# Performance work log

Hardware: AMD Instinct MI355X
Metric: run time of the kernel (lower is better)

Reference implementation:

```python
import jax, jax.numpy as jnp
import numpy as np

EPS = 1e-5


def setup_inputs() -> dict:
    key = jax.random.key(0)
    k1, k2, k3, k4 = jax.random.split(key, 4)
    B, C, H, W = 32, 256, 64, 64
    x_real = jax.random.normal(k1, (B, C, H, W), dtype=jnp.float32)
    x_imag = jax.random.normal(k2, (B, C, H, W), dtype=jnp.float32)
    # per-channel 2x2 affine weight and 2-vector bias (module init is
    # 0.7071*I and zeros; we perturb so gradients are non-trivial)
    weight = (0.70710678 * jnp.eye(2, dtype=jnp.float32)[:, :, None]
              + 0.05 * jax.random.normal(k3, (2, 2, C), dtype=jnp.float32))
    bias = 0.05 * jax.random.normal(k4, (2, C), dtype=jnp.float32)
    return {"x_real": x_real, "x_imag": x_imag, "weight": weight, "bias": bias}


def reference(x_real, x_imag, weight, bias):
    # Complex BatchNorm (training-mode batch statistics).
    # x_*: [B, C, H, W]; stats reduced over (B, H, W) per channel C.
    axes = (0, 2, 3)
    mu_r = jnp.mean(x_real, axes)  # [C]
    mu_i = jnp.mean(x_imag, axes)  # [C]
    xr = x_real - mu_r[None, :, None, None]
    xi = x_imag - mu_i[None, :, None, None]

    # 2x2 covariance per channel, eps on the diagonal
    Vrr = jnp.mean(xr * xr, axes) + EPS  # [C]
    Vii = jnp.mean(xi * xi, axes) + EPS  # [C]
    Vri = jnp.mean(xr * xi, axes)        # [C]

    # Analytic inverse square root of the 2x2 SPD matrix [[Vrr,Vri],[Vri,Vii]]
    s = jnp.sqrt(Vrr * Vii - Vri * Vri)       # sqrt(det)
    t = jnp.sqrt(Vrr + Vii + 2.0 * s)         # sqrt(trace + 2 sqrt(det))
    inv_st = 1.0 / (s * t)
    Rrr = (Vii + s) * inv_st
    Rii = (Vrr + s) * inv_st
    Rri = -Vri * inv_st

    # Whitening (per-channel 2x2 matmul on (real, imag))
    cb = lambda v: v[None, :, None, None]
    xhat_r = cb(Rrr) * xr + cb(Rri) * xi
    xhat_i = cb(Rri) * xr + cb(Rii) * xi

    # Affine: out = W @ xhat + b, W: [2,2,C], b: [2,C]
    out_r = cb(weight[0, 0]) * xhat_r + cb(weight[0, 1]) * xhat_i + cb(bias[0])
    out_i = cb(weight[1, 0]) * xhat_r + cb(weight[1, 1]) * xhat_i + cb(bias[1])
    return jnp.stack([out_r, out_i], axis=0)  # [2, B, C, H, W]
```

## Files before the change

### kernel.cpp

```cpp
#include <hip/hip_runtime.h>
#include <math.h>

#define C_CH   256
#define HW     4096
#define B_N    32
#define N_PER_CH (B_N * HW)
#define N_TOT  ((size_t)B_N * C_CH * HW)
#define EPS_BN 1e-5f

#define NT 512
#define RS 22
#define LS 9

typedef float f32x4 __attribute__((ext_vector_type(4)));

__device__ __forceinline__ unsigned pk(float a, float b) {
    unsigned ua = __float_as_uint(a);
    unsigned ub = __float_as_uint(b);
    ua += 0x7fffu + ((ua >> 16) & 1u);
    ub += 0x7fffu + ((ub >> 16) & 1u);
    return (ua >> 16) | (ub & 0xffff0000u);
}
__device__ __forceinline__ float blo(unsigned p) { return __uint_as_float(p << 16); }
__device__ __forceinline__ float bhi(unsigned p) { return __uint_as_float(p & 0xffff0000u); }

__global__ __launch_bounds__(NT, 2) void cbn_bf16ret3(
    const float* __restrict__ xr, const float* __restrict__ xi,
    const float* __restrict__ weight,
    const float* __restrict__ bias,
    float* __restrict__ out)
{
    const int c = blockIdx.x;
    const int t = threadIdx.x;

    const f32x4* r4 = reinterpret_cast<const f32x4*>(xr);
    const f32x4* i4 = reinterpret_cast<const f32x4*>(xi);

    __shared__ unsigned lpk[LS][8][NT];
    __shared__ float red[5][NT / 64];
    __shared__ float scoef[6];

    float sr = 0.f, si = 0.f, srr = 0.f, sii = 0.f, sri = 0.f;
    unsigned rp[RS][8];

#define ACC(a, bb)                                              \
    sr  += a.x + a.y + a.z + a.w;                               \
    si  += bb.x + bb.y + bb.z + bb.w;                           \
    srr += a.x*a.x + a.y*a.y + a.z*a.z + a.w*a.w;               \
    sii += bb.x*bb.x + bb.y*bb.y + bb.z*bb.z + bb.w*bb.w;       \
    sri += a.x*bb.x + a.y*bb.y + a.z*bb.z + a.w*bb.w;

#pragma unroll
    for (int j = 0; j < RS; ++j) {
        const size_t base = ((size_t)(j * C_CH + c) << 10);
        const f32x4 a0 = __builtin_nontemporal_load(&r4[base + t]);
        const f32x4 a1 = __builtin_nontemporal_load(&r4[base + NT + t]);
        const f32x4 b0 = __builtin_nontemporal_load(&i4[base + t]);
        const f32x4 b1 = __builtin_nontemporal_load(&i4[base + NT + t]);
        rp[j][0] = pk(a0.x, a0.y); rp[j][1] = pk(a0.z, a0.w);
        rp[j][2] = pk(a1.x, a1.y); rp[j][3] = pk(a1.z, a1.w);
        rp[j][4] = pk(b0.x, b0.y); rp[j][5] = pk(b0.z, b0.w);
        rp[j][6] = pk(b1.x, b1.y); rp[j][7] = pk(b1.z, b1.w);
        ACC(a0, b0) ACC(a1, b1)
    }
#pragma unroll
    for (int j = 0; j < LS; ++j) {
        const size_t base = ((size_t)((RS + j) * C_CH + c) << 10);
        const f32x4 a0 = __builtin_nontemporal_load(&r4[base + t]);
        const f32x4 a1 = __builtin_nontemporal_load(&r4[base + NT + t]);
        const f32x4 b0 = __builtin_nontemporal_load(&i4[base + t]);
        const f32x4 b1 = __builtin_nontemporal_load(&i4[base + NT + t]);
        lpk[j][0][t] = pk(a0.x, a0.y); lpk[j][1][t] = pk(a0.z, a0.w);
        lpk[j][2][t] = pk(a1.x, a1.y); lpk[j][3][t] = pk(a1.z, a1.w);
        lpk[j][4][t] = pk(b0.x, b0.y); lpk[j][5][t] = pk(b0.z, b0.w);
        lpk[j][6][t] = pk(b1.x, b1.y); lpk[j][7][t] = pk(b1.z, b1.w);
        ACC(a0, b0) ACC(a1, b1)
    }
    {
        const size_t base = ((size_t)((B_N - 1) * C_CH + c) << 10);
        const f32x4 a0 = r4[base + t];
        const f32x4 a1 = r4[base + NT + t];
        const f32x4 b0 = i4[base + t];
        const f32x4 b1 = i4[base + NT + t];
        ACC(a0, b0) ACC(a1, b1)
    }
#undef ACC

#pragma unroll
    for (int off = 32; off > 0; off >>= 1) {
        sr  += __shfl_down(sr,  off);
        si  += __shfl_down(si,  off);
        srr += __shfl_down(srr, off);
        sii += __shfl_down(sii, off);
        sri += __shfl_down(sri, off);
    }
    const int wave = t >> 6;
    if ((t & 63) == 0) {
        red[0][wave] = sr;  red[1][wave] = si;
        red[2][wave] = srr; red[3][wave] = sii; red[4][wave] = sri;
    }
    __syncthreads();

    if (t == 0) {
        float v[5];
#pragma unroll
        for (int k = 0; k < 5; ++k) {
            float acc = red[k][0];
#pragma unroll
            for (int w = 1; w < NT / 64; ++w) acc += red[k][w];
            v[k] = acc;
        }
        const float invN = 1.0f / (float)N_PER_CH;
        const float mur = v[0] * invN;
        const float mui = v[1] * invN;
        const float Vrr = v[2] * invN - mur * mur + EPS_BN;
        const float Vii = v[3] * invN - mui * mui + EPS_BN;
        const float Vri = v[4] * invN - mur * mui;

        const float s      = sqrtf(Vrr * Vii - Vri * Vri);
        const float tt     = sqrtf(Vrr + Vii + 2.0f * s);
        const float inv_st = 1.0f / (s * tt);
        const float Rrr = (Vii + s) * inv_st;
        const float Rii = (Vrr + s) * inv_st;
        const float Rri = -Vri * inv_st;

        const float w00 = weight[0 * C_CH + c];
        const float w01 = weight[1 * C_CH + c];
        const float w10 = weight[2 * C_CH + c];
        const float w11 = weight[3 * C_CH + c];
        const float b0  = bias[c];
        const float b1  = bias[C_CH + c];

        const float Ar = w00 * Rrr + w01 * Rri;
        const float Br = w00 * Rri + w01 * Rii;
        const float Ai = w10 * Rrr + w11 * Rri;
        const float Bi = w10 * Rri + w11 * Rii;

        scoef[0] = Ar;
        scoef[1] = Br;
        scoef[2] = b0 - Ar * mur - Br * mui;
        scoef[3] = Ai;
        scoef[4] = Bi;
        scoef[5] = b1 - Ai * mur - Bi * mui;
    }
    __syncthreads();

    const float Ar = scoef[0], Br = scoef[1], Cr = scoef[2];
    const float Ai = scoef[3], Bi = scoef[4], Ci = scoef[5];

    f32x4* o4 = reinterpret_cast<f32x4*>(out);
    const size_t n4 = N_TOT / 4;

#define APPLY_STORE(a, bb, idx)                                    \
    {   f32x4 u, w_;                                               \
        u.x = Ar*a.x + Br*bb.x + Cr;  u.y = Ar*a.y + Br*bb.y + Cr; \
        u.z = Ar*a.z + Br*bb.z + Cr;  u.w = Ar*a.w + Br*bb.w + Cr; \
        w_.x = Ai*a.x + Bi*bb.x + Ci; w_.y = Ai*a.y + Bi*bb.y + Ci;\
        w_.z = Ai*a.z + Bi*bb.z + Ci; w_.w = Ai*a.w + Bi*bb.w + Ci;\
        __builtin_nontemporal_store(u,  &o4[idx]);                 \
        __builtin_nontemporal_store(w_, &o4[n4 + idx]); }

#define UNPK(p0, p1, dst) { dst.x = blo(p0); dst.y = bhi(p0); dst.z = blo(p1); dst.w = bhi(p1); }

    {
        const size_t base = ((size_t)((B_N - 1) * C_CH + c) << 10);
        const f32x4 a0 = r4[base + t];
        const f32x4 a1 = r4[base + NT + t];
        const f32x4 b0 = i4[base + t];
        const f32x4 b1 = i4[base + NT + t];
        APPLY_STORE(a0, b0, base + t)
        APPLY_STORE(a1, b1, base + NT + t)
    }
#pragma unroll
    for (int j = 0; j < LS; ++j) {
        const size_t base = ((size_t)((RS + j) * C_CH + c) << 10);
        f32x4 a0, a1, b0, b1;
        UNPK(lpk[j][0][t], lpk[j][1][t], a0)
        UNPK(lpk[j][2][t], lpk[j][3][t], a1)
        UNPK(lpk[j][4][t], lpk[j][5][t], b0)
        UNPK(lpk[j][6][t], lpk[j][7][t], b1)
        APPLY_STORE(a0, b0, base + t)
        APPLY_STORE(a1, b1, base + NT + t)
    }
#pragma unroll
    for (int j = 0; j < RS; ++j) {
        const size_t base = ((size_t)(j * C_CH + c) << 10);
        f32x4 a0, a1, b0, b1;
        UNPK(rp[j][0], rp[j][1], a0)
        UNPK(rp[j][2], rp[j][3], a1)
        UNPK(rp[j][4], rp[j][5], b0)
        UNPK(rp[j][6], rp[j][7], b1)
        APPLY_STORE(a0, b0, base + t)
        APPLY_STORE(a1, b1, base + NT + t)
    }
#undef APPLY_STORE
#undef UNPK
}

extern "C" void kernel_launch(void* const* d_in, const int* in_sizes, int n_in,
                              void* d_out, int out_size, void* d_ws, size_t ws_size,
                              hipStream_t stream) {
    const float* xr     = (const float*)d_in[0];
    const float* xi     = (const float*)d_in[1];
    const float* weight = (const float*)d_in[2];
    const float* bias   = (const float*)d_in[3];
    float* out = (float*)d_out;

    cbn_bf16ret3<<<C_CH, NT, 0, stream>>>(xr, xi, weight, bias, out);
}
```

Measured before the change: 112.7 us.

## Split each channel across two cooperating blocks with flag-based partial-stat exchange

Each channel is now handled by two blocks, each covering half the batch, for 512 blocks total instead of 256. The pair exchanges partial sums through workspace memory, using a release/acquire flag and a spin-wait. Per-block register and LDS retention shrink, and launch bounds move to 4 blocks per CU, with the aim of raising occupancy and filling all CUs. The spin-wait relies on both blocks of a pair being co-resident, so it risks deadlock if that does not hold, and it adds a memset launch per call.

```diff
diff --git a/kernel.cpp b/kernel.cpp
--- a/kernel.cpp
+++ b/kernel.cpp
@@ -9,8 +9,9 @@
 #define EPS_BN 1e-5f
 
 #define NT 512
-#define RS 22
-#define LS 9
+#define HALF 16
+#define RS 9
+#define LS 4
 
 typedef float f32x4 __attribute__((ext_vector_type(4)));
 
@@ -24,14 +25,19 @@
 __device__ __forceinline__ float blo(unsigned p) { return __uint_as_float(p << 16); }
 __device__ __forceinline__ float bhi(unsigned p) { return __uint_as_float(p & 0xffff0000u); }
 
-__global__ __launch_bounds__(NT, 2) void cbn_bf16ret3(
+__global__ __launch_bounds__(NT, 4) void cbn_dual(
     const float* __restrict__ xr, const float* __restrict__ xi,
     const float* __restrict__ weight,
     const float* __restrict__ bias,
-    float* __restrict__ out)
+    float* __restrict__ out,
+    float* __restrict__ part,
+    int*   __restrict__ flag)
 {
-    const int c = blockIdx.x;
-    const int t = threadIdx.x;
+    const int b  = blockIdx.x;
+    const int c  = b >> 1;
+    const int h  = b & 1;
+    const int t  = threadIdx.x;
+    const int j0 = h * HALF;
 
     const f32x4* r4 = reinterpret_cast<const f32x4*>(xr);
     const f32x4* i4 = reinterpret_cast<const f32x4*>(xi);
@@ -52,7 +58,7 @@
 
 #pragma unroll
     for (int j = 0; j < RS; ++j) {
-        const size_t base = ((size_t)(j * C_CH + c) << 10);
+        const size_t base = ((size_t)((j0 + j) * C_CH + c) << 10);
         const f32x4 a0 = __builtin_nontemporal_load(&r4[base + t]);
         const f32x4 a1 = __builtin_nontemporal_load(&r4[base + NT + t]);
         const f32x4 b0 = __builtin_nontemporal_load(&i4[base + t]);
@@ -65,7 +71,7 @@
     }
 #pragma unroll
     for (int j = 0; j < LS; ++j) {
-        const size_t base = ((size_t)((RS + j) * C_CH + c) << 10);
+        const size_t base = ((size_t)((j0 + RS + j) * C_CH + c) << 10);
         const f32x4 a0 = __builtin_nontemporal_load(&r4[base + t]);
         const f32x4 a1 = __builtin_nontemporal_load(&r4[base + NT + t]);
         const f32x4 b0 = __builtin_nontemporal_load(&i4[base + t]);
@@ -76,8 +82,9 @@
         lpk[j][6][t] = pk(b1.x, b1.y); lpk[j][7][t] = pk(b1.z, b1.w);
         ACC(a0, b0) ACC(a1, b1)
     }
-    {
-        const size_t base = ((size_t)((B_N - 1) * C_CH + c) << 10);
+#pragma unroll
+    for (int j = RS + LS; j < HALF; ++j) {
+        const size_t base = ((size_t)((j0 + j) * C_CH + c) << 10);
         const f32x4 a0 = r4[base + t];
         const f32x4 a1 = r4[base + NT + t];
         const f32x4 b0 = i4[base + t];
@@ -102,14 +109,34 @@
     __syncthreads();
 
     if (t == 0) {
-        float v[5];
+        float own[5];
 #pragma unroll
         for (int k = 0; k < 5; ++k) {
             float acc = red[k][0];
 #pragma unroll
             for (int w = 1; w < NT / 64; ++w) acc += red[k][w];
-            v[k] = acc;
+            own[k] = acc;
         }
+#pragma unroll
+        for (int k = 0; k < 5; ++k)
+            __hip_atomic_store(&part[b * 5 + k], own[k],
+                               __ATOMIC_RELAXED, __HIP_MEMORY_SCOPE_AGENT);
+        __hip_atomic_store(&flag[b], 1,
+                           __ATOMIC_RELEASE, __HIP_MEMORY_SCOPE_AGENT);
+
+        const int ob = b ^ 1;
+        while (__hip_atomic_load(&flag[ob],
+                                 __ATOMIC_ACQUIRE, __HIP_MEMORY_SCOPE_AGENT) == 0) {
+            __builtin_amdgcn_s_sleep(8);
+        }
+        float v[5];
+#pragma unroll
+        for (int k = 0; k < 5; ++k) {
+            const float oth = __hip_atomic_load(&part[ob * 5 + k],
+                                                __ATOMIC_RELAXED, __HIP_MEMORY_SCOPE_AGENT);
+            v[k] = own[k] + oth;
+        }
+
         const float invN = 1.0f / (float)N_PER_CH;
         const float mur = v[0] * invN;
         const float mui = v[1] * invN;
@@ -162,8 +189,9 @@
 
 #define UNPK(p0, p1, dst) { dst.x = blo(p0); dst.y = bhi(p0); dst.z = blo(p1); dst.w = bhi(p1); }
 
-    {
-        const size_t base = ((size_t)((B_N - 1) * C_CH + c) << 10);
+#pragma unroll
+    for (int j = RS + LS; j < HALF; ++j) {
+        const size_t base = ((size_t)((j0 + j) * C_CH + c) << 10);
         const f32x4 a0 = r4[base + t];
         const f32x4 a1 = r4[base + NT + t];
         const f32x4 b0 = i4[base + t];
@@ -173,7 +201,7 @@
     }
 #pragma unroll
     for (int j = 0; j < LS; ++j) {
-        const size_t base = ((size_t)((RS + j) * C_CH + c) << 10);
+        const size_t base = ((size_t)((j0 + RS + j) * C_CH + c) << 10);
         f32x4 a0, a1, b0, b1;
         UNPK(lpk[j][0][t], lpk[j][1][t], a0)
         UNPK(lpk[j][2][t], lpk[j][3][t], a1)
@@ -184,7 +212,7 @@
     }
 #pragma unroll
     for (int j = 0; j < RS; ++j) {
-        const size_t base = ((size_t)(j * C_CH + c) << 10);
+        const size_t base = ((size_t)((j0 + j) * C_CH + c) << 10);
         f32x4 a0, a1, b0, b1;
         UNPK(rp[j][0], rp[j][1], a0)
         UNPK(rp[j][2], rp[j][3], a1)
@@ -206,5 +234,10 @@
     const float* bias   = (const float*)d_in[3];
     float* out = (float*)d_out;
 
-    cbn_bf16ret3<<<C_CH, NT, 0, stream>>>(xr, xi, weight, bias, out);
+    int*   flag = (int*)d_ws;
+    float* part = (float*)((char*)d_ws + 2048);
+
+    hipMemsetAsync(d_ws, 0, 2048, stream);
+
+    cbn_dual<<<512, NT, 0, stream>>>(xr, xi, weight, bias, out, part, flag);
 }
```

After: 144.4 us. 1.28x slower.
